# Optimization experiments

Hardware: AMD Instinct MI355X
Metric: run time of the kernel (lower is better)

## Reference

```python
import jax, jax.numpy as jnp
import numpy as np

K = 256
Q = 64
T = 500001  # length of return series r


def setup_inputs() -> dict:
    key = jax.random.key(0)
    k_r, k_b, k_w0, k_w = jax.random.split(key, 4)
    r = 0.01 * jax.random.normal(k_r, (T,), dtype=jnp.float32)
    a0 = jnp.float32(0.0)
    a1 = jnp.float32(0.0)
    raw_beta0 = jnp.float32(-4.0)
    raw_beta = (-4.0 + 0.1 * jax.random.normal(k_b, (K,))).astype(jnp.float32)
    raw_w0 = (-8.0 + 0.1 * jax.random.normal(k_w0, (K,))).astype(jnp.float32)
    raw_w = (-4.0 + 0.1 * jax.random.normal(k_w, (K, Q))).astype(jnp.float32)
    return {"r": r, "a0": a0, "a1": a1, "raw_beta0": raw_beta0,
            "raw_beta": raw_beta, "raw_w0": raw_w0, "raw_w": raw_w}


def reference(r, a0, a1, raw_beta0, raw_beta, raw_w0, raw_w):
    # AR(1) residuals
    u = r[1:] - a0 - a1 * r[:-1]          # [T-1]
    u2 = u * u                            # [T-1]
    n = u.shape[0]
    # init_u2 = unbiased variance of u2, repeated q times (torch.var default ddof=1)
    init_u2 = jnp.full((Q,), jnp.var(u2, ddof=1), dtype=u2.dtype)
    u2_full = jnp.concatenate([init_u2, u2])  # [q + T-1]
    # vectorized windowing: row t holds u2_full[t+q-1], ..., u2_full[t] (flipped window)
    t_idx = jnp.arange(n)[:, None]        # [n,1]
    lag_idx = jnp.arange(Q)[None, :]      # [1,q]
    idx = (Q + t_idx) - 1 - lag_idx       # [n,q]
    u2_lags = u2_full[idx]                # [n,q]
    # softplus-MLP volatility
    w0 = jax.nn.softplus(raw_w0)          # [k]
    w = jax.nn.softplus(raw_w)            # [k,q]
    h = jax.nn.relu(w0[None, :] + u2_lags @ w.T)  # [n,k]
    beta0 = jax.nn.softplus(raw_beta0)
    beta = jax.nn.softplus(raw_beta)      # [k]
    sigma2 = beta0 + h @ beta + 1e-8      # [n]
    # Gaussian negative log-likelihood
    nll = (0.5 * n * jnp.log(jnp.float32(2.0 * np.pi))
           + 0.5 * jnp.sum(jnp.log(sigma2))
           + 0.5 * jnp.sum(u2 / sigma2))
    return nll
```

## Files before the change

### kernel.cpp

```cpp
#include <hip/hip_runtime.h>
#include <math.h>

#define K_ 256
#define Q_ 64
#define NT 500000
#define TPB 1024
#define NBLK_F 489
#define GRID_MAIN 489

#define WS_C0    2
#define WS_U2    4
#define WS_V     (WS_U2 + Q_ + NT)
#define WS_PART  (WS_V + Q_)
#define WS_PART2 (WS_PART + 512)
#define WS_OUT   (WS_PART2 + 512)

typedef __attribute__((ext_vector_type(4))) float f32x4;

__device__ __forceinline__ float softplusf(float x) {
    return (x > 20.f) ? x : log1pf(__expf(x));
}

__global__ void k_front(const float* __restrict__ r,
                        const float* __restrict__ a0p,
                        const float* __restrict__ a1p,
                        const float* __restrict__ raw_beta0,
                        const float* __restrict__ raw_beta,
                        const float* __restrict__ raw_w0,
                        const float* __restrict__ raw_w,
                        float* __restrict__ ws) {
    __shared__ float red[8];
    __shared__ float sbeta[K_];
    __shared__ f32x4 vpart[16][16];
    __shared__ float cred[4];
    int tid = threadIdx.x;

    if (blockIdx.x < NBLK_F) {
        int i0 = 4 * (blockIdx.x * 256 + tid);
        float a0 = a0p[0], a1 = a1p[0];
        float v = 0.f, v2 = 0.f;
        if (i0 + 7 <= NT) {
            f32x4 ra = *(const f32x4*)(r + i0);
            f32x4 rb = *(const f32x4*)(r + i0 + 4);
            float u0 = ra[1] - a0 - a1 * ra[0];
            float u1 = ra[2] - a0 - a1 * ra[1];
            float u2 = ra[3] - a0 - a1 * ra[2];
            float u3 = rb[0] - a0 - a1 * ra[3];
            f32x4 q; q[0] = u0*u0; q[1] = u1*u1; q[2] = u2*u2; q[3] = u3*u3;
            *(f32x4*)(ws + WS_U2 + Q_ + i0) = q;
            v  = (q[0] + q[1]) + (q[2] + q[3]);
            v2 = (q[0]*q[0] + q[1]*q[1]) + (q[2]*q[2] + q[3]*q[3]);
        } else {
            #pragma unroll
            for (int j = 0; j < 4; ++j) {
                int i = i0 + j;
                if (i < NT) {
                    float u = r[i + 1] - a0 - a1 * r[i];
                    float q = u * u;
                    ws[WS_U2 + Q_ + i] = q;
                    v += q; v2 += q * q;
                }
            }
        }
        #pragma unroll
        for (int off = 32; off > 0; off >>= 1) {
            v  += __shfl_down(v,  off, 64);
            v2 += __shfl_down(v2, off, 64);
        }
        int wv = tid >> 6;
        if ((tid & 63) == 0) { red[wv * 2] = v; red[wv * 2 + 1] = v2; }
        __syncthreads();
        if (tid == 0) {
            ws[WS_PART  + blockIdx.x] = red[0] + red[2] + red[4] + red[6];
            ws[WS_PART2 + blockIdx.x] = red[1] + red[3] + red[5] + red[7];
        }
    } else {
        sbeta[tid] = softplusf(raw_beta[tid]);
        __syncthreads();
        int c = tid >> 4, jq = tid & 15;
        f32x4 wv[16];
        #pragma unroll
        for (int kk = 0; kk < 16; ++kk)
            wv[kk] = *(const f32x4*)(raw_w + (16 * c + kk) * Q_ + 4 * jq);
        f32x4 pv; pv[0] = pv[1] = pv[2] = pv[3] = 0.f;
        #pragma unroll
        for (int kk = 0; kk < 16; ++kk) {
            float bk = sbeta[16 * c + kk];
            pv[0] = fmaf(bk, softplusf(wv[kk][0]), pv[0]);
            pv[1] = fmaf(bk, softplusf(wv[kk][1]), pv[1]);
            pv[2] = fmaf(bk, softplusf(wv[kk][2]), pv[2]);
            pv[3] = fmaf(bk, softplusf(wv[kk][3]), pv[3]);
        }
        vpart[c][jq] = pv;
        float pc = sbeta[tid] * softplusf(raw_w0[tid]);
        #pragma unroll
        for (int mask = 1; mask < 64; mask <<= 1)
            pc += __shfl_xor(pc, mask, 64);
        if ((tid & 63) == 0) cred[tid >> 6] = pc;
        __syncthreads();
        if (tid < Q_) {
            int q = tid >> 2, d = tid & 3;
            float vj = 0.f;
            #pragma unroll
            for (int cc = 0; cc < 16; ++cc) vj += vpart[cc][q][d];
            ws[WS_V + (Q_ - 1 - tid)] = vj;
        }
        if (tid == 0)
            ws[WS_C0] = softplusf(raw_beta0[0])
                      + ((cred[0] + cred[1]) + (cred[2] + cred[3])) + 1e-8f;
    }
}

__launch_bounds__(256)
__global__ void k_main(float* __restrict__ ws) {
    __shared__ __align__(16) float su[TPB + Q_];
    __shared__ float red[4];
    int tid = threadIdx.x;
    int l = tid & 63, w = tid >> 6;

    if (blockIdx.x == 0) {
        if (tid < 64) {
            float s1 = 0.f, s2 = 0.f;
            for (int p = tid; p < NBLK_F; p += 64) {
                s1 += ws[WS_PART  + p];
                s2 += ws[WS_PART2 + p];
            }
            #pragma unroll
            for (int mask = 1; mask < 64; mask <<= 1) {
                s1 += __shfl_xor(s1, mask, 64);
                s2 += __shfl_xor(s2, mask, 64);
            }
            float n   = (float)NT;
            float var = (s2 - s1 * s1 / n) / (n - 1.f);
            ws[WS_U2 + tid] = var;
        }
        __syncthreads();
    }

    int t0 = blockIdx.x * TPB;
    for (int m = tid; m < (TPB + Q_) / 4; m += 256)
        *(f32x4*)(su + 4 * m) = *(const f32x4*)(ws + WS_U2 + t0 + 4 * m);

    float c0v = ws[WS_C0];
    f32x4 vr4[16];
    #pragma unroll
    for (int m = 0; m < 16; ++m)
        vr4[m] = *(const f32x4*)(ws + WS_V + 4 * m);
    __syncthreads();

    f32x4 acc; acc[0] = c0v; acc[1] = c0v; acc[2] = c0v; acc[3] = c0v;
    const float* sw = su + 4 * tid;
    f32x4 cur = *(const f32x4*)sw;
    #pragma unroll
    for (int m = 0; m < 16; ++m) {
        f32x4 nxt = *(const f32x4*)(sw + 4 * m + 4);
        #pragma unroll
        for (int d = 0; d < 4; ++d) {
            float vv = vr4[m][d];
            acc[0] = fmaf(cur[d], vv, acc[0]);
            acc[1] = fmaf(d < 3 ? cur[d + 1] : nxt[d - 3], vv, acc[1]);
            acc[2] = fmaf(d < 2 ? cur[d + 2] : nxt[d - 2], vv, acc[2]);
            acc[3] = fmaf(d < 1 ? cur[d + 3] : nxt[d - 1], vv, acc[3]);
        }
        cur = nxt;
    }

    int t = t0 + 4 * tid;
    f32x4 u4 = *(const f32x4*)(ws + WS_U2 + Q_ + t);
    float val = 0.f;
    #pragma unroll
    for (int j = 0; j < 4; ++j)
        if (t + j < NT) val += __logf(acc[j]) + u4[j] / acc[j];

    #pragma unroll
    for (int mask = 1; mask < 64; mask <<= 1)
        val += __shfl_xor(val, mask, 64);
    if (l == 0) red[w] = val;
    __syncthreads();
    if (tid == 0)
        ws[WS_OUT + blockIdx.x] = (red[0] + red[1]) + (red[2] + red[3]);
}

__global__ void k_final(const float* __restrict__ ws, float* __restrict__ out) {
    __shared__ float red[4];
    int tid = threadIdx.x;
    float s = 0.f;
    for (int p = tid; p < GRID_MAIN; p += 256) s += ws[WS_OUT + p];
    #pragma unroll
    for (int mask = 1; mask < 64; mask <<= 1)
        s += __shfl_xor(s, mask, 64);
    if ((tid & 63) == 0) red[tid >> 6] = s;
    __syncthreads();
    if (tid == 0)
        out[0] = 0.5f * (float)NT * 1.8378770664093453f
               + 0.5f * ((red[0] + red[1]) + (red[2] + red[3]));
}

extern "C" void kernel_launch(void* const* d_in, const int* in_sizes, int n_in,
                              void* d_out, int out_size, void* d_ws, size_t ws_size,
                              hipStream_t stream) {
    const float* r        = (const float*)d_in[0];
    const float* a0       = (const float*)d_in[1];
    const float* a1       = (const float*)d_in[2];
    const float* raw_b0   = (const float*)d_in[3];
    const float* raw_beta = (const float*)d_in[4];
    const float* raw_w0   = (const float*)d_in[5];
    const float* raw_w    = (const float*)d_in[6];
    float* out = (float*)d_out;
    float* ws  = (float*)d_ws;

    k_front<<<NBLK_F + 1, 256, 0, stream>>>(
        r, a0, a1, raw_b0, raw_beta, raw_w0, raw_w, ws);

    k_main<<<GRID_MAIN, 256, 0, stream>>>(ws);

    k_final<<<1, 256, 0, stream>>>(ws, out);
}
```

Before: 91.43 us.

## Fuse front and main kernels, defer variance-dependent first-window correction to final

Merges the residual/variance pass and the convolution pass into one kernel. Each block recomputes the squared residuals for its window directly from r into shared memory, and recomputes the softplus weight vector locally. This removes the u2 round trip through global memory and one kernel launch. The variance-dependent init padding only affects the first 64 outputs, so those positions are computed with zeros and later corrected linearly in the final kernel. Each thread now covers 8 outputs with a larger tile (2048 per block), which adds redundant per-block weight computation and raises register pressure.

```diff
diff --git a/kernel.cpp b/kernel.cpp
--- a/kernel.cpp
+++ b/kernel.cpp
@@ -4,16 +4,15 @@
 #define K_ 256
 #define Q_ 64
 #define NT 500000
-#define TPB 1024
-#define NBLK_F 489
-#define GRID_MAIN 489
-
-#define WS_C0    2
-#define WS_U2    4
-#define WS_V     (WS_U2 + Q_ + NT)
-#define WS_PART  (WS_V + Q_)
-#define WS_PART2 (WS_PART + 512)
-#define WS_OUT   (WS_PART2 + 512)
+#define TPB 2048
+#define GRID_MAIN ((NT + TPB - 1) / TPB)
+
+#define WS_PART  0
+#define WS_PART2 (WS_PART + 256)
+#define WS_OUT   (WS_PART2 + 256)
+#define WS_SG64  (WS_OUT + 256)
+#define WS_U264  (WS_SG64 + 64)
+#define WS_VR    (WS_U264 + 64)
 
 typedef __attribute__((ext_vector_type(4))) float f32x4;
 
@@ -21,175 +20,195 @@
     return (x > 20.f) ? x : log1pf(__expf(x));
 }
 
-__global__ void k_front(const float* __restrict__ r,
-                        const float* __restrict__ a0p,
-                        const float* __restrict__ a1p,
-                        const float* __restrict__ raw_beta0,
-                        const float* __restrict__ raw_beta,
-                        const float* __restrict__ raw_w0,
-                        const float* __restrict__ raw_w,
-                        float* __restrict__ ws) {
-    __shared__ float red[8];
+__launch_bounds__(256)
+__global__ void k_main(const float* __restrict__ r,
+                       const float* __restrict__ a0p,
+                       const float* __restrict__ a1p,
+                       const float* __restrict__ rb0,
+                       const float* __restrict__ rbeta,
+                       const float* __restrict__ rw0,
+                       const float* __restrict__ rw,
+                       float* __restrict__ ws) {
+    __shared__ __align__(16) float su[TPB + Q_];
     __shared__ float sbeta[K_];
-    __shared__ f32x4 vpart[16][16];
-    __shared__ float cred[4];
+    __shared__ __align__(16) f32x4 vpart[16][16];
+    __shared__ __align__(16) float vrs[Q_];
+    __shared__ float sc0s;
+    __shared__ float red[4][3];
     int tid = threadIdx.x;
-
-    if (blockIdx.x < NBLK_F) {
-        int i0 = 4 * (blockIdx.x * 256 + tid);
-        float a0 = a0p[0], a1 = a1p[0];
-        float v = 0.f, v2 = 0.f;
-        if (i0 + 7 <= NT) {
-            f32x4 ra = *(const f32x4*)(r + i0);
-            f32x4 rb = *(const f32x4*)(r + i0 + 4);
+    int l = tid & 63, w = tid >> 6;
+    float a0 = a0p[0], a1 = a1p[0];
+    int t0 = blockIdx.x * TPB;
+    int base = t0 - Q_;
+
+    sbeta[tid] = softplusf(rbeta[tid]);
+
+    int c = tid >> 4, jq = tid & 15;
+    f32x4 wv[16];
+    #pragma unroll
+    for (int kk = 0; kk < 16; ++kk)
+        wv[kk] = *(const f32x4*)(rw + (16 * c + kk) * Q_ + 4 * jq);
+
+    float v = 0.f, v2 = 0.f;
+    for (int qd = tid; qd < (TPB + Q_) / 4; qd += 256) {
+        int m = 4 * qd;
+        int j = base + m;
+        f32x4 qv;
+        if (j >= 0 && j + 8 <= NT + 1) {
+            f32x4 ra = *(const f32x4*)(r + j);
+            f32x4 rb = *(const f32x4*)(r + j + 4);
             float u0 = ra[1] - a0 - a1 * ra[0];
             float u1 = ra[2] - a0 - a1 * ra[1];
             float u2 = ra[3] - a0 - a1 * ra[2];
             float u3 = rb[0] - a0 - a1 * ra[3];
-            f32x4 q; q[0] = u0*u0; q[1] = u1*u1; q[2] = u2*u2; q[3] = u3*u3;
-            *(f32x4*)(ws + WS_U2 + Q_ + i0) = q;
-            v  = (q[0] + q[1]) + (q[2] + q[3]);
-            v2 = (q[0]*q[0] + q[1]*q[1]) + (q[2]*q[2] + q[3]*q[3]);
+            qv[0] = u0*u0; qv[1] = u1*u1; qv[2] = u2*u2; qv[3] = u3*u3;
         } else {
             #pragma unroll
-            for (int j = 0; j < 4; ++j) {
-                int i = i0 + j;
-                if (i < NT) {
-                    float u = r[i + 1] - a0 - a1 * r[i];
-                    float q = u * u;
-                    ws[WS_U2 + Q_ + i] = q;
-                    v += q; v2 += q * q;
+            for (int d = 0; d < 4; ++d) {
+                int je = j + d;
+                float q = 0.f;
+                if (je >= 0 && je < NT) {
+                    float u = r[je + 1] - a0 - a1 * r[je];
+                    q = u * u;
                 }
+                qv[d] = q;
             }
         }
+        *(f32x4*)(su + m) = qv;
+        if (m >= Q_) {
+            v  += (qv[0] + qv[1]) + (qv[2] + qv[3]);
+            v2 += (qv[0]*qv[0] + qv[1]*qv[1]) + (qv[2]*qv[2] + qv[3]*qv[3]);
+        }
+    }
+    __syncthreads();
+
+    f32x4 pv; pv[0] = pv[1] = pv[2] = pv[3] = 0.f;
+    #pragma unroll
+    for (int kk = 0; kk < 16; ++kk) {
+        float bk = sbeta[16 * c + kk];
+        pv[0] = fmaf(bk, softplusf(wv[kk][0]), pv[0]);
+        pv[1] = fmaf(bk, softplusf(wv[kk][1]), pv[1]);
+        pv[2] = fmaf(bk, softplusf(wv[kk][2]), pv[2]);
+        pv[3] = fmaf(bk, softplusf(wv[kk][3]), pv[3]);
+    }
+    vpart[c][jq] = pv;
+    float pc = sbeta[tid] * softplusf(rw0[tid]);
+    #pragma unroll
+    for (int mask = 1; mask < 64; mask <<= 1)
+        pc += __shfl_xor(pc, mask, 64);
+    if (l == 0) red[w][0] = pc;
+    __syncthreads();
+
+    if (tid < Q_) {
+        int qq = tid >> 2, dd = tid & 3;
+        float vj = 0.f;
         #pragma unroll
-        for (int off = 32; off > 0; off >>= 1) {
-            v  += __shfl_down(v,  off, 64);
-            v2 += __shfl_down(v2, off, 64);
-        }
-        int wv = tid >> 6;
-        if ((tid & 63) == 0) { red[wv * 2] = v; red[wv * 2 + 1] = v2; }
-        __syncthreads();
-        if (tid == 0) {
-            ws[WS_PART  + blockIdx.x] = red[0] + red[2] + red[4] + red[6];
-            ws[WS_PART2 + blockIdx.x] = red[1] + red[3] + red[5] + red[7];
-        }
-    } else {
-        sbeta[tid] = softplusf(raw_beta[tid]);
-        __syncthreads();
-        int c = tid >> 4, jq = tid & 15;
-        f32x4 wv[16];
+        for (int cc = 0; cc < 16; ++cc) vj += vpart[cc][qq][dd];
+        vrs[Q_ - 1 - tid] = vj;
+        if (blockIdx.x == 0) ws[WS_VR + (Q_ - 1 - tid)] = vj;
+    }
+    if (tid == 0)
+        sc0s = softplusf(rb0[0])
+             + ((red[0][0] + red[1][0]) + (red[2][0] + red[3][0])) + 1e-8f;
+    __syncthreads();
+
+    float c0v = sc0s;
+    float acc[8];
+    #pragma unroll
+    for (int jj = 0; jj < 8; ++jj) acc[jj] = c0v;
+    f32x4 vr4[16];
+    #pragma unroll
+    for (int mc = 0; mc < 16; ++mc)
+        vr4[mc] = *(const f32x4*)(vrs + 4 * mc);
+    const float* sw = su + 8 * tid;
+    f32x4 A = *(const f32x4*)(sw);
+    f32x4 B = *(const f32x4*)(sw + 4);
+    #pragma unroll
+    for (int mc = 0; mc < 16; ++mc) {
+        f32x4 C = *(const f32x4*)(sw + 4 * mc + 8);
         #pragma unroll
-        for (int kk = 0; kk < 16; ++kk)
-            wv[kk] = *(const f32x4*)(raw_w + (16 * c + kk) * Q_ + 4 * jq);
-        f32x4 pv; pv[0] = pv[1] = pv[2] = pv[3] = 0.f;
+        for (int d = 0; d < 4; ++d) {
+            float vv = vr4[mc][d];
+            #pragma unroll
+            for (int jj = 0; jj < 8; ++jj) {
+                int idx = d + jj;
+                float x = idx < 4 ? A[idx] : (idx < 8 ? B[idx - 4] : C[idx - 8]);
+                acc[jj] = fmaf(x, vv, acc[jj]);
+            }
+        }
+        A = B; B = C;
+    }
+
+    float val = 0.f;
+    int tb = t0 + 8 * tid;
+    #pragma unroll
+    for (int jj = 0; jj < 8; ++jj) {
+        int t = tb + jj;
+        float sg = acc[jj];
+        if (t >= Q_ && t < NT) {
+            float u2t = su[8 * tid + jj + Q_];
+            val += __logf(sg) + u2t / sg;
+        }
+    }
+    if (blockIdx.x == 0 && tid < 8) {
         #pragma unroll
-        for (int kk = 0; kk < 16; ++kk) {
-            float bk = sbeta[16 * c + kk];
-            pv[0] = fmaf(bk, softplusf(wv[kk][0]), pv[0]);
-            pv[1] = fmaf(bk, softplusf(wv[kk][1]), pv[1]);
-            pv[2] = fmaf(bk, softplusf(wv[kk][2]), pv[2]);
-            pv[3] = fmaf(bk, softplusf(wv[kk][3]), pv[3]);
-        }
-        vpart[c][jq] = pv;
-        float pc = sbeta[tid] * softplusf(raw_w0[tid]);
-        #pragma unroll
-        for (int mask = 1; mask < 64; mask <<= 1)
-            pc += __shfl_xor(pc, mask, 64);
-        if ((tid & 63) == 0) cred[tid >> 6] = pc;
-        __syncthreads();
-        if (tid < Q_) {
-            int q = tid >> 2, d = tid & 3;
-            float vj = 0.f;
-            #pragma unroll
-            for (int cc = 0; cc < 16; ++cc) vj += vpart[cc][q][d];
-            ws[WS_V + (Q_ - 1 - tid)] = vj;
-        }
-        if (tid == 0)
-            ws[WS_C0] = softplusf(raw_beta0[0])
-                      + ((cred[0] + cred[1]) + (cred[2] + cred[3])) + 1e-8f;
-    }
-}
-
-__launch_bounds__(256)
-__global__ void k_main(float* __restrict__ ws) {
-    __shared__ __align__(16) float su[TPB + Q_];
-    __shared__ float red[4];
+        for (int jj = 0; jj < 8; ++jj) {
+            int t = 8 * tid + jj;
+            ws[WS_SG64 + t] = acc[jj];
+            ws[WS_U264 + t] = su[8 * tid + jj + Q_];
+        }
+    }
+
+    #pragma unroll
+    for (int mask = 1; mask < 64; mask <<= 1) {
+        v   += __shfl_xor(v,   mask, 64);
+        v2  += __shfl_xor(v2,  mask, 64);
+        val += __shfl_xor(val, mask, 64);
+    }
+    if (l == 0) { red[w][0] = v; red[w][1] = v2; red[w][2] = val; }
+    __syncthreads();
+    if (tid == 0) {
+        ws[WS_PART  + blockIdx.x] = (red[0][0] + red[1][0]) + (red[2][0] + red[3][0]);
+        ws[WS_PART2 + blockIdx.x] = (red[0][1] + red[1][1]) + (red[2][1] + red[3][1]);
+        ws[WS_OUT   + blockIdx.x] = (red[0][2] + red[1][2]) + (red[2][2] + red[3][2]);
+    }
+}
+
+__global__ void k_final(const float* __restrict__ ws, float* __restrict__ out) {
+    __shared__ float svr[Q_];
+    __shared__ float r1[4], r2[4], red[4];
     int tid = threadIdx.x;
     int l = tid & 63, w = tid >> 6;
 
-    if (blockIdx.x == 0) {
-        if (tid < 64) {
-            float s1 = 0.f, s2 = 0.f;
-            for (int p = tid; p < NBLK_F; p += 64) {
-                s1 += ws[WS_PART  + p];
-                s2 += ws[WS_PART2 + p];
-            }
-            #pragma unroll
-            for (int mask = 1; mask < 64; mask <<= 1) {
-                s1 += __shfl_xor(s1, mask, 64);
-                s2 += __shfl_xor(s2, mask, 64);
-            }
-            float n   = (float)NT;
-            float var = (s2 - s1 * s1 / n) / (n - 1.f);
-            ws[WS_U2 + tid] = var;
-        }
-        __syncthreads();
-    }
-
-    int t0 = blockIdx.x * TPB;
-    for (int m = tid; m < (TPB + Q_) / 4; m += 256)
-        *(f32x4*)(su + 4 * m) = *(const f32x4*)(ws + WS_U2 + t0 + 4 * m);
-
-    float c0v = ws[WS_C0];
-    f32x4 vr4[16];
-    #pragma unroll
-    for (int m = 0; m < 16; ++m)
-        vr4[m] = *(const f32x4*)(ws + WS_V + 4 * m);
-    __syncthreads();
-
-    f32x4 acc; acc[0] = c0v; acc[1] = c0v; acc[2] = c0v; acc[3] = c0v;
-    const float* sw = su + 4 * tid;
-    f32x4 cur = *(const f32x4*)sw;
-    #pragma unroll
-    for (int m = 0; m < 16; ++m) {
-        f32x4 nxt = *(const f32x4*)(sw + 4 * m + 4);
-        #pragma unroll
-        for (int d = 0; d < 4; ++d) {
-            float vv = vr4[m][d];
-            acc[0] = fmaf(cur[d], vv, acc[0]);
-            acc[1] = fmaf(d < 3 ? cur[d + 1] : nxt[d - 3], vv, acc[1]);
-            acc[2] = fmaf(d < 2 ? cur[d + 2] : nxt[d - 2], vv, acc[2]);
-            acc[3] = fmaf(d < 1 ? cur[d + 3] : nxt[d - 1], vv, acc[3]);
-        }
-        cur = nxt;
-    }
-
-    int t = t0 + 4 * tid;
-    f32x4 u4 = *(const f32x4*)(ws + WS_U2 + Q_ + t);
+    float s1 = (tid < GRID_MAIN) ? ws[WS_PART  + tid] : 0.f;
+    float s2 = (tid < GRID_MAIN) ? ws[WS_PART2 + tid] : 0.f;
+    float so = (tid < GRID_MAIN) ? ws[WS_OUT   + tid] : 0.f;
+    if (tid < Q_) svr[tid] = ws[WS_VR + tid];
+
+    #pragma unroll
+    for (int mask = 1; mask < 64; mask <<= 1) {
+        s1 += __shfl_xor(s1, mask, 64);
+        s2 += __shfl_xor(s2, mask, 64);
+    }
+    if (l == 0) { r1[w] = s1; r2[w] = s2; }
+    __syncthreads();
+    float S1 = (r1[0] + r1[1]) + (r1[2] + r1[3]);
+    float S2 = (r2[0] + r2[1]) + (r2[2] + r2[3]);
+    float n = (float)NT;
+    float var = (S2 - S1 * S1 / n) / (n - 1.f);
+
     float val = 0.f;
-    #pragma unroll
-    for (int j = 0; j < 4; ++j)
-        if (t + j < NT) val += __logf(acc[j]) + u4[j] / acc[j];
-
+    if (tid < Q_) {
+        float cs = 0.f;
+        for (int e = 0; e < Q_ - tid; ++e) cs += svr[e];
+        float sg = ws[WS_SG64 + tid] + var * cs;
+        val = __logf(sg) + ws[WS_U264 + tid] / sg;
+    }
+    float tot = so + val;
     #pragma unroll
     for (int mask = 1; mask < 64; mask <<= 1)
-        val += __shfl_xor(val, mask, 64);
-    if (l == 0) red[w] = val;
-    __syncthreads();
-    if (tid == 0)
-        ws[WS_OUT + blockIdx.x] = (red[0] + red[1]) + (red[2] + red[3]);
-}
-
-__global__ void k_final(const float* __restrict__ ws, float* __restrict__ out) {
-    __shared__ float red[4];
-    int tid = threadIdx.x;
-    float s = 0.f;
-    for (int p = tid; p < GRID_MAIN; p += 256) s += ws[WS_OUT + p];
-    #pragma unroll
-    for (int mask = 1; mask < 64; mask <<= 1)
-        s += __shfl_xor(s, mask, 64);
-    if ((tid & 63) == 0) red[tid >> 6] = s;
+        tot += __shfl_xor(tot, mask, 64);
+    if (l == 0) red[w] = tot;
     __syncthreads();
     if (tid == 0)
         out[0] = 0.5f * (float)NT * 1.8378770664093453f
@@ -209,10 +228,8 @@
     float* out = (float*)d_out;
     float* ws  = (float*)d_ws;
 
-    k_front<<<NBLK_F + 1, 256, 0, stream>>>(
+    k_main<<<GRID_MAIN, 256, 0, stream>>>(
         r, a0, a1, raw_b0, raw_beta, raw_w0, raw_w, ws);
 
-    k_main<<<GRID_MAIN, 256, 0, stream>>>(ws);
-
     k_final<<<1, 256, 0, stream>>>(ws, out);
 }
```

Result: no change. 91.68 us (+0.3%).
